# Optimization experiments

Hardware: AMD Instinct MI355X
Metric: run time of the kernel (lower is better)

The kernel has to match this reference:

```python
import jax, jax.numpy as jnp
import numpy as np

B, S, D = 1, 2048, 2048
H, HKV, HD = 16, 8, 128
WINDOW = 1024
EPS = 1e-6
SCALE = HD ** -0.5


def _rope_tables(seq_len, head_dim, theta=10000.0):
    inv_freq = 1.0 / (theta ** (jnp.arange(0, head_dim, 2, dtype=jnp.float32) / head_dim))
    ang = jnp.arange(seq_len, dtype=jnp.float32)[:, None] * inv_freq[None, :]  # [S, hd/2]
    emb = jnp.concatenate([ang, ang], axis=-1)  # [S, hd]
    return jnp.cos(emb)[None], jnp.sin(emb)[None]  # [1, S, hd]


def setup_inputs() -> dict:
    key = jax.random.key(0)
    ks = jax.random.split(key, 8)
    cos, sin = _rope_tables(S, HD)
    return {
        "hidden_states": jax.random.normal(ks[0], (B, S, D), jnp.float32),
        "cos": jnp.broadcast_to(cos, (B, S, HD)),
        "sin": jnp.broadcast_to(sin, (B, S, HD)),
        "Wq": jax.random.normal(ks[1], (D, H * HD), jnp.float32) * (D ** -0.5),
        "Wk": jax.random.normal(ks[2], (D, HKV * HD), jnp.float32) * (D ** -0.5),
        "Wv": jax.random.normal(ks[3], (D, HKV * HD), jnp.float32) * (D ** -0.5),
        "Wo": jax.random.normal(ks[4], (H * HD, D), jnp.float32) * ((H * HD) ** -0.5),
        "q_scale": jax.random.uniform(ks[5], (HD,), jnp.float32, 0.5, 1.5),
        "k_scale": jax.random.uniform(ks[6], (HD,), jnp.float32, 0.5, 1.5),
    }


def _rms_norm(x, scale):
    # per-head RMSNorm over last dim, computed in fp32 (matches RMSNorm module)
    xf = x.astype(jnp.float32)
    var = jnp.mean(xf * xf, axis=-1, keepdims=True)
    return (xf * jax.lax.rsqrt(var + EPS) * scale).astype(x.dtype)


def _rotate_half(x):
    x1, x2 = x[..., : HD // 2], x[..., HD // 2 :]
    return jnp.concatenate([-x2, x1], axis=-1)


def _apply_rope(x, cos, sin):
    # cos/sin: [B,S,hd] -> [B,S,1,hd] (unsqueeze_dim=2)
    c, s = cos[:, :, None, :], sin[:, :, None, :]
    return x * c + _rotate_half(x) * s


def reference(hidden_states, cos, sin, Wq, Wk, Wv, Wo, q_scale, k_scale):
    b, s, _ = hidden_states.shape
    q = (hidden_states @ Wq).reshape(b, s, H, HD)
    k = (hidden_states @ Wk).reshape(b, s, HKV, HD)
    v = (hidden_states @ Wv).reshape(b, s, HKV, HD)
    q = _rms_norm(q, q_scale)
    k = _rms_norm(k, k_scale)
    q = _apply_rope(q, cos, sin)
    k = _apply_rope(k, cos, sin)
    # GQA: repeat kv heads to match query heads (groups are consecutive)
    g = H // HKV
    k = jnp.repeat(k, g, axis=2)  # [b, s, H, hd]
    v = jnp.repeat(v, g, axis=2)
    scores = jnp.einsum("bqhd,bkhd->bhqk", q, k) * SCALE  # [b,H,S,S]
    i = jnp.arange(s)[:, None]
    j = jnp.arange(s)[None, :]
    allowed = (j <= i) & (i - j <= WINDOW)  # causal + sliding window
    scores = jnp.where(allowed[None, None], scores, -jnp.inf)
    attn = jax.nn.softmax(scores, axis=-1)
    out = jnp.einsum("bhqk,bkhd->bqhd", attn, v).reshape(b, s, H * HD)
    return out @ Wo
```

## Files before the change

kernel.cpp:

```cpp
#include <hip/hip_runtime.h>
#include <hip/hip_bf16.h>
#include <cmath>


typedef __bf16 bf16x8 __attribute__((ext_vector_type(8)));
typedef float  f32x4  __attribute__((ext_vector_type(4)));

#define S_LEN    2048
#define NH       16
#define NKV      8
#define HDIM     128
#define WIN      1024
#define QK_SCALE_L2E 0.12751744595f
#define RMS_EPS  1e-6f

__device__ __forceinline__ void gld16(void* lds, const void* g) {
    __builtin_amdgcn_global_load_lds(
        (const __attribute__((address_space(1))) unsigned int*)g,
        (__attribute__((address_space(3))) unsigned int*)lds, 16, 0, 0);
}

__device__ __forceinline__ unsigned short f2bu(float x) {
    __hip_bfloat16 h = __float2bfloat16(x);
    return *(unsigned short*)&h;
}

__global__ __launch_bounds__(256) void cvt_hs_kernel(
    const float* __restrict__ src, __hip_bfloat16* __restrict__ dst)
{
    size_t i = ((size_t)blockIdx.x * 256 + threadIdx.x) * 8;
    float4 a = *(const float4*)(src + i);
    float4 b = *(const float4*)(src + i + 4);
    unsigned short u[8] = { f2bu(a.x), f2bu(a.y), f2bu(a.z), f2bu(a.w),
                            f2bu(b.x), f2bu(b.y), f2bu(b.z), f2bu(b.w) };
    *(uint4*)(dst + i) = *(uint4*)u;
}

__global__ __launch_bounds__(256) void transpose_w_kernel(
    const float* __restrict__ Wq, const float* __restrict__ Wk,
    const float* __restrict__ Wv, const float* __restrict__ Wo,
    __hip_bfloat16* __restrict__ WqkvT, __hip_bfloat16* __restrict__ WoT)
{
    __shared__ __attribute__((aligned(16))) unsigned short tile[64][72];
    int id = blockIdx.x;
    const float* src; __hip_bfloat16* dst; int N, kt, nt;
    if (id < 1024)      { src = Wq; dst = WqkvT;                          N = 2048; kt = id >> 5;          nt = id & 31; }
    else if (id < 1536) { src = Wk; dst = WqkvT + (size_t)2048*2048;      N = 1024; kt = (id-1024) >> 4;   nt = (id-1024) & 15; }
    else if (id < 2048) { src = Wv; dst = WqkvT + (size_t)3072*2048;      N = 1024; kt = (id-1536) >> 4;   nt = (id-1536) & 15; }
    else                { src = Wo; dst = WoT;                            N = 2048; kt = (id-2048) >> 5;   nt = (id-2048) & 31; }
    int k0 = kt * 64, n0 = nt * 64;
    int tid = threadIdx.x;
#pragma unroll
    for (int p = 0; p < 2; ++p) {
        int c = p*256 + tid; int r = c >> 3, cc = (c & 7) * 8;
        const float* s = src + (size_t)(k0 + r)*N + n0 + cc;
        float4 a = *(const float4*)s;
        float4 b = *(const float4*)(s + 4);
        unsigned short u[8] = { f2bu(a.x), f2bu(a.y), f2bu(a.z), f2bu(a.w),
                                f2bu(b.x), f2bu(b.y), f2bu(b.z), f2bu(b.w) };
        *(uint4*)&tile[r][cc] = *(uint4*)u;
    }
    __syncthreads();
#pragma unroll
    for (int p = 0; p < 2; ++p) {
        int c = p*256 + tid; int r2 = c >> 3, c2 = (c & 7) * 8;
        uint4 o;
        o.x = tile[c2+0][r2] | ((unsigned)tile[c2+1][r2] << 16);
        o.y = tile[c2+2][r2] | ((unsigned)tile[c2+3][r2] << 16);
        o.z = tile[c2+4][r2] | ((unsigned)tile[c2+5][r2] << 16);
        o.w = tile[c2+6][r2] | ((unsigned)tile[c2+7][r2] << 16);
        *(uint4*)(dst + (size_t)(n0 + r2)*2048 + k0 + c2) = o;
    }
}

__global__ __launch_bounds__(256) void vtrans_kernel(
    const __hip_bfloat16* __restrict__ qkv, __hip_bfloat16* __restrict__ Vt)
{
    __shared__ __attribute__((aligned(16))) unsigned short tile[64][72];
    int s0 = blockIdx.x * 64;
    int v0 = blockIdx.y * 64;
    int tid = threadIdx.x;
#pragma unroll
    for (int p = 0; p < 2; ++p) {
        int c = p*256 + tid; int r = c >> 3, cc = (c & 7) * 8;
        uint4 v = *(const uint4*)(qkv + (size_t)(s0 + r)*4096 + 3072 + v0 + cc);
        *(uint4*)&tile[r][cc] = v;
    }
    __syncthreads();
#pragma unroll
    for (int p = 0; p < 2; ++p) {
        int c = p*256 + tid; int r2 = c >> 3, c2 = (c & 7) * 8;
        uint4 o;
        o.x = tile[c2+0][r2] | ((unsigned)tile[c2+1][r2] << 16);
        o.y = tile[c2+2][r2] | ((unsigned)tile[c2+3][r2] << 16);
        o.z = tile[c2+4][r2] | ((unsigned)tile[c2+5][r2] << 16);
        o.w = tile[c2+6][r2] | ((unsigned)tile[c2+7][r2] << 16);
        *(uint4*)(Vt + (size_t)(v0 + r2)*2048 + s0 + c2) = o;
    }
}

template <typename OT>
__global__ __launch_bounds__(256) void gemm_bt_kernel(
    const __hip_bfloat16* __restrict__ A, const __hip_bfloat16* __restrict__ BT,
    OT* __restrict__ C, int M, int N, int K)
{
    __shared__ __attribute__((aligned(16))) __hip_bfloat16 As[128*32];
    __shared__ __attribute__((aligned(16))) __hip_bfloat16 Bs[128*32];
    const int tid  = threadIdx.x;
    const int lane = tid & 63;
    const int wave = tid >> 6;
    const int quad = lane >> 4, l15 = lane & 15;
    const int m0 = blockIdx.y * 128, n0 = blockIdx.x * 128;
    const int wm = (wave >> 1) * 64, wn = (wave & 1) * 64;

    f32x4 acc[4][4] = {};

    for (int k0 = 0; k0 < K; k0 += 32) {
#pragma unroll
        for (int p = 0; p < 2; ++p) {
            int c = p*256 + tid;
            int row = c >> 2, seg = c & 3;
            gld16((char*)As + c*16, A  + (size_t)(m0 + row)*K + k0 + seg*8);
            gld16((char*)Bs + c*16, BT + (size_t)(n0 + row)*K + k0 + seg*8);
        }
        __syncthreads();
        bf16x8 af[4], bfr[4];
#pragma unroll
        for (int t = 0; t < 4; ++t) {
            af[t]  = *(const bf16x8*)(As + (wm + t*16 + l15)*32 + quad*8);
            bfr[t] = *(const bf16x8*)(Bs + (wn + t*16 + l15)*32 + quad*8);
        }
#pragma unroll
        for (int mt = 0; mt < 4; ++mt)
#pragma unroll
            for (int nt = 0; nt < 4; ++nt)
                acc[mt][nt] = __builtin_amdgcn_mfma_f32_16x16x32_bf16(af[mt], bfr[nt], acc[mt][nt], 0, 0, 0);
        __syncthreads();
    }
#pragma unroll
    for (int mt = 0; mt < 4; ++mt)
#pragma unroll
        for (int nt = 0; nt < 4; ++nt)
#pragma unroll
            for (int r = 0; r < 4; ++r) {
                int row = m0 + wm + mt*16 + quad*4 + r;
                int col = n0 + wn + nt*16 + l15;
                if constexpr (__is_same(OT, float))
                    C[(size_t)row*N + col] = acc[mt][nt][r];
                else
                    C[(size_t)row*N + col] = __float2bfloat16(acc[mt][nt][r]);
            }
}

__global__ __launch_bounds__(256) void rmsrope_kernel(
    const __hip_bfloat16* __restrict__ qkv,
    const float* __restrict__ cosb, const float* __restrict__ sinb,
    const float* __restrict__ qsc,  const float* __restrict__ ksc,
    __hip_bfloat16* __restrict__ Qn, __hip_bfloat16* __restrict__ Kn)
{
    int s = blockIdx.x;
    int wave = threadIdx.x >> 6, lane = threadIdx.x & 63;
    float c1 = cosb[s*128 + lane];
    float c2 = cosb[s*128 + 64 + lane];
    float s1 = sinb[s*128 + lane];
    float s2 = sinb[s*128 + 64 + lane];
    for (int u = wave; u < 24; u += 4) {
        bool isq = (u < 16);
        int h = isq ? u : u - 16;
        const __hip_bfloat16* x = qkv + (size_t)s*4096 + (isq ? h*128 : 2048 + h*128);
        float x1 = (float)x[lane], x2 = (float)x[lane + 64];
        float ss = x1*x1 + x2*x2;
#pragma unroll
        for (int off = 32; off; off >>= 1) ss += __shfl_xor(ss, off);
        float r = rsqrtf(ss * (1.0f/128.0f) + RMS_EPS);
        if (isq) r *= QK_SCALE_L2E;
        const float* sc = isq ? qsc : ksc;
        float y1 = x1 * r * sc[lane];
        float y2 = x2 * r * sc[lane + 64];
        float o1 = y1*c1 - y2*s1;
        float o2 = y2*c2 + y1*s2;
        __hip_bfloat16* dst = isq ? (Qn + (size_t)s*2048 + h*128)
                                  : (Kn + (size_t)s*1024 + h*128);
        dst[lane]      = __float2bfloat16(o1);
        dst[lane + 64] = __float2bfloat16(o2);
    }
}

__global__ __launch_bounds__(256, 2) void attn_kernel(
    const __hip_bfloat16* __restrict__ Qn,
    const __hip_bfloat16* __restrict__ Kn,
    const __hip_bfloat16* __restrict__ Vt,
    __hip_bfloat16* __restrict__ O)
{
    __shared__ __attribute__((aligned(16))) __hip_bfloat16 Ksm[2][64*128];
    __shared__ __attribute__((aligned(16))) __hip_bfloat16 Vsm[2][128*64];
    __shared__ __attribute__((aligned(16))) __hip_bfloat16 P[4][16][76];

    const int bx   = blockIdx.x;
    const int h    = bx & 15;
    const int qb   = 31 - (bx >> 4);
    const int i0   = qb * 64;
    const int hk   = h >> 1;
    const int tid  = threadIdx.x, wave = tid >> 6, lane = tid & 63;
    const int quad = lane >> 4, l15 = lane & 15;
    const int ib   = i0 + wave * 16;

    const __hip_bfloat16* Kh = Kn + hk * HDIM;
    const __hip_bfloat16* Vh = Vt + (size_t)(hk * HDIM) * 2048;

    bf16x8 qf[4];
    const __hip_bfloat16* qbase = Qn + (size_t)(ib + l15)*2048 + h*HDIM + quad*8;
#pragma unroll
    for (int kk = 0; kk < 4; ++kk) qf[kk] = *(const bf16x8*)(qbase + kk*32);

    f32x4 o[8] = {};
    float lrow[4] = {0.f, 0.f, 0.f, 0.f};

    int j_lo = i0 - WIN; if (j_lo < 0) j_lo = 0;
    const int jstart = j_lo & ~63;
    const int jend   = i0;

    auto stage = [&](int b, int j0) {
#pragma unroll
        for (int p = 0; p < 4; ++p) {
            int L = p*256 + tid;
            int r = L >> 4;
            int c = (L & 15) ^ (r & 15);
            gld16((char*)&Ksm[b][0] + L*16, Kh + (size_t)(j0 + r)*1024 + c*8);
        }
#pragma unroll
        for (int p = 0; p < 4; ++p) {
            int L = p*256 + tid;
            int dv = L >> 3;
            int c = (L & 7) ^ (dv & 7);
            gld16((char*)&Vsm[b][0] + L*16, Vh + (size_t)dv*2048 + j0 + c*8);
        }
    };

    stage(0, jstart);
    int cur = 0;
    for (int j0 = jstart; j0 <= jend; j0 += 64, cur ^= 1) {
        __syncthreads();
        if (j0 + 64 <= jend) stage(cur ^ 1, j0 + 64);

        f32x4 sacc[4] = {};
#pragma unroll
        for (int nt = 0; nt < 4; ++nt) {
            const int r = nt*16 + l15;
#pragma unroll
            for (int kk = 0; kk < 4; ++kk) {
                const int cc = (kk*4 + quad) ^ l15;
                bf16x8 kfr = *(const bf16x8*)(&Ksm[cur][0] + r*128 + cc*8);
                sacc[nt] = __builtin_amdgcn_mfma_f32_16x16x32_bf16(qf[kk], kfr, sacc[nt], 0, 0, 0);
            }
        }

        const bool need_mask = (j0 + 63 > ib) || (j0 < ib + 15 - WIN);
        if (need_mask) {
#pragma unroll
            for (int nt = 0; nt < 4; ++nt) {
                int j = j0 + nt*16 + l15;
#pragma unroll
                for (int r = 0; r < 4; ++r) {
                    int i = ib + quad*4 + r;
                    bool valid = (j <= i) && (i - j <= WIN);
                    float p = valid ? __builtin_exp2f(sacc[nt][r]) : 0.f;
                    lrow[r] += p;
                    P[wave][quad*4 + r][nt*16 + l15] = __float2bfloat16(p);
                }
            }
        } else {
#pragma unroll
            for (int nt = 0; nt < 4; ++nt)
#pragma unroll
                for (int r = 0; r < 4; ++r) {
                    float p = __builtin_exp2f(sacc[nt][r]);
                    lrow[r] += p;
                    P[wave][quad*4 + r][nt*16 + l15] = __float2bfloat16(p);
                }
        }

#pragma unroll
        for (int ks = 0; ks < 2; ++ks) {
            bf16x8 pf = *(const bf16x8*)&P[wave][l15][ks*32 + quad*8];
#pragma unroll
            for (int dt = 0; dt < 8; ++dt) {
                const int dv = dt*16 + l15;
                const int cc = (ks*4 + quad) ^ (l15 & 7);
                bf16x8 vfr = *(const bf16x8*)(&Vsm[cur][0] + dv*64 + cc*8);
                o[dt] = __builtin_amdgcn_mfma_f32_16x16x32_bf16(pf, vfr, o[dt], 0, 0, 0);
            }
        }
    }

#pragma unroll
    for (int r = 0; r < 4; ++r) {
        lrow[r] += __shfl_xor(lrow[r], 1);
        lrow[r] += __shfl_xor(lrow[r], 2);
        lrow[r] += __shfl_xor(lrow[r], 4);
        lrow[r] += __shfl_xor(lrow[r], 8);
        float inv = 1.0f / lrow[r];
        int row = ib + quad*4 + r;
#pragma unroll
        for (int dt = 0; dt < 8; ++dt)
            O[(size_t)row*2048 + h*HDIM + dt*16 + l15] = __float2bfloat16(o[dt][r] * inv);
    }
}

extern "C" void kernel_launch(void* const* d_in, const int* in_sizes, int n_in,
                              void* d_out, int out_size, void* d_ws, size_t ws_size,
                              hipStream_t stream)
{
    (void)in_sizes; (void)n_in; (void)out_size; (void)ws_size;
    const float* hs   = (const float*)d_in[0];
    const float* cosb = (const float*)d_in[1];
    const float* sinb = (const float*)d_in[2];
    const float* Wq   = (const float*)d_in[3];
    const float* Wk   = (const float*)d_in[4];
    const float* Wv   = (const float*)d_in[5];
    const float* Wo   = (const float*)d_in[6];
    const float* qs   = (const float*)d_in[7];
    const float* ks   = (const float*)d_in[8];

    char* ws = (char*)d_ws;
    __hip_bfloat16* WqkvT = (__hip_bfloat16*)(ws);
    __hip_bfloat16* WoT   = (__hip_bfloat16*)(ws + (16u << 20));
    __hip_bfloat16* QKV   = (__hip_bfloat16*)(ws + (24u << 20));
    __hip_bfloat16* Qn    = (__hip_bfloat16*)(ws + (40u << 20));
    __hip_bfloat16* Kn    = (__hip_bfloat16*)(ws + (48u << 20));
    __hip_bfloat16* Vt    = (__hip_bfloat16*)(ws + (52u << 20));
    __hip_bfloat16* hsb   = (__hip_bfloat16*)(ws + (56u << 20));
    __hip_bfloat16* AT    = (__hip_bfloat16*)(ws + (56u << 20));

    cvt_hs_kernel<<<dim3(2048), dim3(256), 0, stream>>>(hs, hsb);
    transpose_w_kernel<<<dim3(3072), dim3(256), 0, stream>>>(Wq, Wk, Wv, Wo, WqkvT, WoT);
    gemm_bt_kernel<__hip_bfloat16><<<dim3(32, 16), dim3(256), 0, stream>>>(hsb, WqkvT, QKV, 2048, 4096, 2048);
    rmsrope_kernel<<<dim3(2048), dim3(256), 0, stream>>>(QKV, cosb, sinb, qs, ks, Qn, Kn);
    vtrans_kernel<<<dim3(32, 16), dim3(256), 0, stream>>>(QKV, Vt);
    attn_kernel<<<dim3(512), dim3(256), 0, stream>>>(Qn, Kn, Vt, AT);
    gemm_bt_kernel<float><<<dim3(16, 16), dim3(256), 0, stream>>>(AT, WoT, (float*)d_out, 2048, 2048, 2048);
}
```

Before: 261.6 us.

## Merge prep kernels and swizzle GEMM LDS layout to avoid bank conflicts

Folds the hidden-state fp32-to-bf16 conversion into the weight transpose launch and the V transpose into the RMSNorm/RoPE launch, reducing kernel launches and tail gaps. Adds an XOR swizzle to the LDS tile layout in the bf16 GEMM so MFMA fragment reads hit different banks. Merged kernels carry branchy block roles and share the LDS allocation with blocks that do not need it.

```diff
diff --git a/kernel.cpp b/kernel.cpp
--- a/kernel.cpp
+++ b/kernel.cpp
@@ -25,24 +25,24 @@
     return *(unsigned short*)&h;
 }
 
-__global__ __launch_bounds__(256) void cvt_hs_kernel(
-    const float* __restrict__ src, __hip_bfloat16* __restrict__ dst)
-{
-    size_t i = ((size_t)blockIdx.x * 256 + threadIdx.x) * 8;
-    float4 a = *(const float4*)(src + i);
-    float4 b = *(const float4*)(src + i + 4);
-    unsigned short u[8] = { f2bu(a.x), f2bu(a.y), f2bu(a.z), f2bu(a.w),
-                            f2bu(b.x), f2bu(b.y), f2bu(b.z), f2bu(b.w) };
-    *(uint4*)(dst + i) = *(uint4*)u;
-}
-
-__global__ __launch_bounds__(256) void transpose_w_kernel(
+__global__ __launch_bounds__(256) void trans_cvt_kernel(
     const float* __restrict__ Wq, const float* __restrict__ Wk,
     const float* __restrict__ Wv, const float* __restrict__ Wo,
-    __hip_bfloat16* __restrict__ WqkvT, __hip_bfloat16* __restrict__ WoT)
+    const float* __restrict__ hs,
+    __hip_bfloat16* __restrict__ WqkvT, __hip_bfloat16* __restrict__ WoT,
+    __hip_bfloat16* __restrict__ hsb)
 {
     __shared__ __attribute__((aligned(16))) unsigned short tile[64][72];
     int id = blockIdx.x;
+    if (id >= 3072) {
+        size_t i = ((size_t)(id - 3072) * 256 + threadIdx.x) * 8;
+        float4 a = *(const float4*)(hs + i);
+        float4 b = *(const float4*)(hs + i + 4);
+        unsigned short u[8] = { f2bu(a.x), f2bu(a.y), f2bu(a.z), f2bu(a.w),
+                                f2bu(b.x), f2bu(b.y), f2bu(b.z), f2bu(b.w) };
+        *(uint4*)(hsb + i) = *(uint4*)u;
+        return;
+    }
     const float* src; __hip_bfloat16* dst; int N, kt, nt;
     if (id < 1024)      { src = Wq; dst = WqkvT;                          N = 2048; kt = id >> 5;          nt = id & 31; }
     else if (id < 1536) { src = Wk; dst = WqkvT + (size_t)2048*2048;      N = 1024; kt = (id-1024) >> 4;   nt = (id-1024) & 15; }
@@ -73,32 +73,6 @@
     }
 }
 
-__global__ __launch_bounds__(256) void vtrans_kernel(
-    const __hip_bfloat16* __restrict__ qkv, __hip_bfloat16* __restrict__ Vt)
-{
-    __shared__ __attribute__((aligned(16))) unsigned short tile[64][72];
-    int s0 = blockIdx.x * 64;
-    int v0 = blockIdx.y * 64;
-    int tid = threadIdx.x;
-#pragma unroll
-    for (int p = 0; p < 2; ++p) {
-        int c = p*256 + tid; int r = c >> 3, cc = (c & 7) * 8;
-        uint4 v = *(const uint4*)(qkv + (size_t)(s0 + r)*4096 + 3072 + v0 + cc);
-        *(uint4*)&tile[r][cc] = v;
-    }
-    __syncthreads();
-#pragma unroll
-    for (int p = 0; p < 2; ++p) {
-        int c = p*256 + tid; int r2 = c >> 3, c2 = (c & 7) * 8;
-        uint4 o;
-        o.x = tile[c2+0][r2] | ((unsigned)tile[c2+1][r2] << 16);
-        o.y = tile[c2+2][r2] | ((unsigned)tile[c2+3][r2] << 16);
-        o.z = tile[c2+4][r2] | ((unsigned)tile[c2+5][r2] << 16);
-        o.w = tile[c2+6][r2] | ((unsigned)tile[c2+7][r2] << 16);
-        *(uint4*)(Vt + (size_t)(v0 + r2)*2048 + s0 + c2) = o;
-    }
-}
-
 template <typename OT>
 __global__ __launch_bounds__(256) void gemm_bt_kernel(
     const __hip_bfloat16* __restrict__ A, const __hip_bfloat16* __restrict__ BT,
@@ -112,6 +86,7 @@
     const int quad = lane >> 4, l15 = lane & 15;
     const int m0 = blockIdx.y * 128, n0 = blockIdx.x * 128;
     const int wm = (wave >> 1) * 64, wn = (wave & 1) * 64;
+    const int sw = (quad ^ ((l15 >> 1) & 3)) * 8;
 
     f32x4 acc[4][4] = {};
 
@@ -120,15 +95,16 @@
         for (int p = 0; p < 2; ++p) {
             int c = p*256 + tid;
             int row = c >> 2, seg = c & 3;
-            gld16((char*)As + c*16, A  + (size_t)(m0 + row)*K + k0 + seg*8);
-            gld16((char*)Bs + c*16, BT + (size_t)(n0 + row)*K + k0 + seg*8);
+            int cs = seg ^ ((row >> 1) & 3);
+            gld16((char*)As + c*16, A  + (size_t)(m0 + row)*K + k0 + cs*8);
+            gld16((char*)Bs + c*16, BT + (size_t)(n0 + row)*K + k0 + cs*8);
         }
         __syncthreads();
         bf16x8 af[4], bfr[4];
 #pragma unroll
         for (int t = 0; t < 4; ++t) {
-            af[t]  = *(const bf16x8*)(As + (wm + t*16 + l15)*32 + quad*8);
-            bfr[t] = *(const bf16x8*)(Bs + (wn + t*16 + l15)*32 + quad*8);
+            af[t]  = *(const bf16x8*)(As + (wm + t*16 + l15)*32 + sw);
+            bfr[t] = *(const bf16x8*)(Bs + (wn + t*16 + l15)*32 + sw);
         }
 #pragma unroll
         for (int mt = 0; mt < 4; ++mt)
@@ -152,13 +128,40 @@
             }
 }
 
-__global__ __launch_bounds__(256) void rmsrope_kernel(
+__global__ __launch_bounds__(256) void rms_vt_kernel(
     const __hip_bfloat16* __restrict__ qkv,
     const float* __restrict__ cosb, const float* __restrict__ sinb,
     const float* __restrict__ qsc,  const float* __restrict__ ksc,
-    __hip_bfloat16* __restrict__ Qn, __hip_bfloat16* __restrict__ Kn)
-{
-    int s = blockIdx.x;
+    __hip_bfloat16* __restrict__ Qn, __hip_bfloat16* __restrict__ Kn,
+    __hip_bfloat16* __restrict__ Vt)
+{
+    __shared__ __attribute__((aligned(16))) unsigned short tile[64][72];
+    int id = blockIdx.x;
+    if (id >= 2048) {
+        int t  = id - 2048;
+        int s0 = (t & 31) * 64;
+        int v0 = (t >> 5) * 64;
+        int tid = threadIdx.x;
+#pragma unroll
+        for (int p = 0; p < 2; ++p) {
+            int c = p*256 + tid; int r = c >> 3, cc = (c & 7) * 8;
+            uint4 v = *(const uint4*)(qkv + (size_t)(s0 + r)*4096 + 3072 + v0 + cc);
+            *(uint4*)&tile[r][cc] = v;
+        }
+        __syncthreads();
+#pragma unroll
+        for (int p = 0; p < 2; ++p) {
+            int c = p*256 + tid; int r2 = c >> 3, c2 = (c & 7) * 8;
+            uint4 o;
+            o.x = tile[c2+0][r2] | ((unsigned)tile[c2+1][r2] << 16);
+            o.y = tile[c2+2][r2] | ((unsigned)tile[c2+3][r2] << 16);
+            o.z = tile[c2+4][r2] | ((unsigned)tile[c2+5][r2] << 16);
+            o.w = tile[c2+6][r2] | ((unsigned)tile[c2+7][r2] << 16);
+            *(uint4*)(Vt + (size_t)(v0 + r2)*2048 + s0 + c2) = o;
+        }
+        return;
+    }
+    int s = id;
     int wave = threadIdx.x >> 6, lane = threadIdx.x & 63;
     float c1 = cosb[s*128 + lane];
     float c2 = cosb[s*128 + 64 + lane];
@@ -332,11 +335,9 @@
     __hip_bfloat16* hsb   = (__hip_bfloat16*)(ws + (56u << 20));
     __hip_bfloat16* AT    = (__hip_bfloat16*)(ws + (56u << 20));
 
-    cvt_hs_kernel<<<dim3(2048), dim3(256), 0, stream>>>(hs, hsb);
-    transpose_w_kernel<<<dim3(3072), dim3(256), 0, stream>>>(Wq, Wk, Wv, Wo, WqkvT, WoT);
+    trans_cvt_kernel<<<dim3(5120), dim3(256), 0, stream>>>(Wq, Wk, Wv, Wo, hs, WqkvT, WoT, hsb);
     gemm_bt_kernel<__hip_bfloat16><<<dim3(32, 16), dim3(256), 0, stream>>>(hsb, WqkvT, QKV, 2048, 4096, 2048);
-    rmsrope_kernel<<<dim3(2048), dim3(256), 0, stream>>>(QKV, cosb, sinb, qs, ks, Qn, Kn);
-    vtrans_kernel<<<dim3(32, 16), dim3(256), 0, stream>>>(QKV, Vt);
+    rms_vt_kernel<<<dim3(2560), dim3(256), 0, stream>>>(QKV, cosb, sinb, qs, ks, Qn, Kn, Vt);
     attn_kernel<<<dim3(512), dim3(256), 0, stream>>>(Qn, Kn, Vt, AT);
     gemm_bt_kernel<float><<<dim3(16, 16), dim3(256), 0, stream>>>(AT, WoT, (float*)d_out, 2048, 2048, 2048);
 }
```

Result: faster. 254.1 us (-2.9%).
